# Optimization experiments

Hardware: AMD Instinct MI355X
Metric: run time of the kernel (lower is better)

Reference implementation:

```python
import jax, jax.numpy as jnp
import numpy as np

B, S, D, H, DFF = 4, 1024, 1024, 16, 4096
DK = D // H
EPS = 1e-9


def _layernorm(x, alpha, bias):
    # Faithful to source: torch.std is unbiased (ddof=1), eps added to std.
    mean = jnp.mean(x, axis=-1, keepdims=True)
    xc = x - mean
    std = jnp.sqrt(jnp.sum(xc * xc, axis=-1, keepdims=True) / (x.shape[-1] - 1))
    return alpha * xc / (std + EPS) + bias


def _mha(x, wq_w, wq_b, wo_w, wo_b):
    # Source bug preserved: w_q is used for q, k, AND v projections.
    p = (x @ wq_w + wq_b).reshape(B, S, H, DK).transpose(0, 2, 1, 3)  # [B,H,S,DK]
    scores = jnp.einsum('bhqd,bhkd->bhqk', p, p) / jnp.sqrt(jnp.asarray(DK, x.dtype))
    attn = jax.nn.softmax(scores, axis=-1)
    out = jnp.einsum('bhqk,bhkd->bhqd', attn, p)
    out = out.transpose(0, 2, 1, 3).reshape(B, S, D)
    return out @ wo_w + wo_b


def _ffn(x, w1, b1, w2, b2):
    return jax.nn.relu(x @ w1 + b1) @ w2 + b2


def setup_inputs() -> dict:
    key = jax.random.key(0)
    ks = jax.random.split(key, 8)
    sc = 0.02
    return {
        'x': jax.random.normal(ks[0], (B, S, D), jnp.float32),
        'wq_w': sc * jax.random.normal(ks[1], (D, D), jnp.float32),
        'wq_b': jnp.zeros((D,), jnp.float32),
        'wo_w': sc * jax.random.normal(ks[2], (D, D), jnp.float32),
        'wo_b': jnp.zeros((D,), jnp.float32),
        'ff1_w': sc * jax.random.normal(ks[3], (D, DFF), jnp.float32),
        'ff1_b': jnp.zeros((DFF,), jnp.float32),
        'ff2_w': sc * jax.random.normal(ks[4], (DFF, D), jnp.float32),
        'ff2_b': jnp.zeros((D,), jnp.float32),
        'alpha1': jnp.ones((1,), jnp.float32), 'bias1': jnp.zeros((1,), jnp.float32),
        'alpha2': jnp.ones((1,), jnp.float32), 'bias2': jnp.zeros((1,), jnp.float32),
        'alpha3': jnp.ones((1,), jnp.float32), 'bias3': jnp.zeros((1,), jnp.float32),
    }


def reference(x, wq_w, wq_b, wo_w, wo_b, ff1_w, ff1_b, ff2_w, ff2_b,
              alpha1, bias1, alpha2, bias2, alpha3, bias3):
    h1 = x + _mha(_layernorm(x, alpha1, bias1), wq_w, wq_b, wo_w, wo_b)
    h2 = h1 + _ffn(_layernorm(h1, alpha2, bias2), ff1_w, ff1_b, ff2_w, ff2_b)
    return _layernorm(h2, alpha3, bias3)
```

## Files before the change

kernel.cpp:

```cpp
#include <hip/hip_runtime.h>

typedef short short8 __attribute__((ext_vector_type(8)));
typedef float f32x4 __attribute__((ext_vector_type(4)));
typedef unsigned short u16x4 __attribute__((ext_vector_type(4)));

#define DEV static __device__ __forceinline__

DEV float b2f(unsigned short u) { return __uint_as_float(((unsigned)u) << 16); }
DEV unsigned short f2b(float f) {
    unsigned u = __float_as_uint(f);
    u += 0x7FFFu + ((u >> 16) & 1u);
    return (unsigned short)(u >> 16);
}
DEV unsigned pack2(float a, float b) {
    return (unsigned)f2b(a) | ((unsigned)f2b(b) << 16);
}
DEV float wred_sum(float v) {
#pragma unroll
    for (int o = 32; o; o >>= 1) v += __shfl_xor(v, o);
    return v;
}

DEV void gld_lds16(const unsigned short* g, unsigned short* l) {
    __builtin_amdgcn_global_load_lds((const __attribute__((address_space(1))) void*)g,
                                     (__attribute__((address_space(3))) void*)l, 16, 0, 0);
}

template <bool OUT_BF16>
__global__ __launch_bounds__(256) void ln_kernel(const float* __restrict__ in,
                                                 void* __restrict__ out_v,
                                                 const float* __restrict__ alpha_p,
                                                 const float* __restrict__ bias_p) {
    __shared__ float redA[4], redB[4];
    const int row = blockIdx.x;
    const int t = threadIdx.x;
    const int lane = t & 63, w = t >> 6;

    f32x4 xv = *(const f32x4*)&in[(size_t)row * 1024 + t * 4];

    float s = wred_sum(xv[0] + xv[1] + xv[2] + xv[3]);
    if (lane == 0) redA[w] = s;
    __syncthreads();
    float mean = (redA[0] + redA[1] + redA[2] + redA[3]) * (1.0f / 1024.0f);

    float d0 = xv[0] - mean, d1 = xv[1] - mean, d2 = xv[2] - mean, d3 = xv[3] - mean;
    float ss = wred_sum(d0 * d0 + d1 * d1 + d2 * d2 + d3 * d3);
    if (lane == 0) redB[w] = ss;
    __syncthreads();
    float var = (redB[0] + redB[1] + redB[2] + redB[3]) * (1.0f / 1023.0f);
    float denom = sqrtf(var) + 1e-9f;
    float inv = alpha_p[0] / denom;
    float bias = bias_p[0];

    if (OUT_BF16) {
        u16x4 o;
        o[0] = f2b(d0 * inv + bias);
        o[1] = f2b(d1 * inv + bias);
        o[2] = f2b(d2 * inv + bias);
        o[3] = f2b(d3 * inv + bias);
        *(u16x4*)&((unsigned short*)out_v)[(size_t)row * 1024 + t * 4] = o;
    } else {
        f32x4 o;
        o[0] = d0 * inv + bias;
        o[1] = d1 * inv + bias;
        o[2] = d2 * inv + bias;
        o[3] = d3 * inv + bias;
        *(f32x4*)&((float*)out_v)[(size_t)row * 1024 + t * 4] = o;
    }
}

__global__ __launch_bounds__(256) void transpose_cast_kernel(const float* __restrict__ in,
                                                             unsigned short* __restrict__ out,
                                                             int R, int C) {
    __shared__ unsigned short tile[32][33];
    const int c0 = blockIdx.x * 32, r0 = blockIdx.y * 32;
    const int x = threadIdx.x, y0 = threadIdx.y;
#pragma unroll
    for (int yy = y0; yy < 32; yy += 8) tile[yy][x] = f2b(in[(size_t)(r0 + yy) * C + c0 + x]);
    __syncthreads();
#pragma unroll
    for (int yy = y0; yy < 32; yy += 8) out[(size_t)(c0 + yy) * R + r0 + x] = tile[x][yy];
}

__global__ __launch_bounds__(256) void transpose_bf16_batch(const unsigned short* __restrict__ in,
                                                            unsigned short* __restrict__ out) {
    __shared__ unsigned short tile[32][33];
    const int b = blockIdx.z;
    const int d0 = blockIdx.x * 32, s0 = blockIdx.y * 32;
    const unsigned short* I = in + (size_t)b * 1024 * 1024;
    unsigned short* O = out + (size_t)b * 1024 * 1024;
    const int x = threadIdx.x, y0 = threadIdx.y;
#pragma unroll
    for (int yy = y0; yy < 32; yy += 8) tile[yy][x] = I[(size_t)(s0 + yy) * 1024 + d0 + x];
    __syncthreads();
#pragma unroll
    for (int yy = y0; yy < 32; yy += 8) O[(size_t)(d0 + yy) * 1024 + s0 + x] = tile[x][yy];
}

template <int BM, int BN, bool RELU, bool RES, bool OUT_BF16>
__global__ __launch_bounds__(256) void gemm2(const unsigned short* __restrict__ A,
                                             const unsigned short* __restrict__ Bt,
                                             const float* __restrict__ bias,
                                             const float* __restrict__ res,
                                             void* __restrict__ C_v,
                                             int M, int N, int K) {
    constexpr int WM = BM / 2, WN = BN / 2;
    constexpr int FM = WM / 16, FN = WN / 16;
    __shared__ __align__(16) unsigned short As[BM * 64];
    __shared__ __align__(16) unsigned short Bs[BN * 64];

    const int t = threadIdx.x;
    const int lane = t & 63, w = t >> 6;
    const int wr = w >> 1, wc = w & 1;
    const int lr = lane & 15, g = lane >> 4;

    const int nwg = gridDim.x;
    const int cpx = nwg >> 3;
    const int wg = blockIdx.x;
    const int swz = (wg & 7) * cpx + (wg >> 3);
    const int NB = N / BN;
    const int m0 = (swz / NB) * BM, n0 = (swz % NB) * BN;

    f32x4 acc[FM][FN];
#pragma unroll
    for (int i = 0; i < FM; ++i)
#pragma unroll
        for (int j = 0; j < FN; ++j) acc[i][j] = (f32x4)0.0f;

    for (int k0 = 0; k0 < K; k0 += 64) {
        __syncthreads();
#pragma unroll
        for (int i = 0; i < BM / 32; ++i) {
            int id = i * 256 + t;
            int row = id >> 3, ch = id & 7;
            gld_lds16(&A[(size_t)(m0 + row) * K + k0 + ((ch ^ (row & 7)) * 8)],
                      &As[(size_t)(i * 256 + (t & ~63)) * 8]);
        }
#pragma unroll
        for (int i = 0; i < BN / 32; ++i) {
            int id = i * 256 + t;
            int row = id >> 3, ch = id & 7;
            gld_lds16(&Bt[(size_t)(n0 + row) * K + k0 + ((ch ^ (row & 7)) * 8)],
                      &Bs[(size_t)(i * 256 + (t & ~63)) * 8]);
        }
        __syncthreads();

        short8 af[FM][2], bfr[FN][2];
#pragma unroll
        for (int mi = 0; mi < FM; ++mi) {
            int row = wr * WM + mi * 16 + lr;
#pragma unroll
            for (int ks = 0; ks < 2; ++ks) {
                int ch = (ks * 4 + g) ^ (row & 7);
                af[mi][ks] = *(const short8*)&As[row * 64 + ch * 8];
            }
        }
#pragma unroll
        for (int ni = 0; ni < FN; ++ni) {
            int row = wc * WN + ni * 16 + lr;
#pragma unroll
            for (int ks = 0; ks < 2; ++ks) {
                int ch = (ks * 4 + g) ^ (row & 7);
                bfr[ni][ks] = *(const short8*)&Bs[row * 64 + ch * 8];
            }
        }
#pragma unroll
        for (int ks = 0; ks < 2; ++ks)
#pragma unroll
            for (int mi = 0; mi < FM; ++mi)
#pragma unroll
                for (int ni = 0; ni < FN; ++ni)
                    acc[mi][ni] = __builtin_amdgcn_mfma_f32_16x16x32_bf16(af[mi][ks], bfr[ni][ks], acc[mi][ni], 0, 0, 0);
    }

    const int lg = g;
#pragma unroll
    for (int ni = 0; ni < FN; ++ni) {
        int col = n0 + wc * WN + ni * 16 + lr;
        float bv = bias[col];
#pragma unroll
        for (int mi = 0; mi < FM; ++mi) {
            int row0 = m0 + wr * WM + mi * 16 + lg * 4;
#pragma unroll
            for (int i = 0; i < 4; ++i) {
                int row = row0 + i;
                float x = acc[mi][ni][i] + bv;
                if (RES) x += res[(size_t)row * N + col];
                if (RELU) x = fmaxf(x, 0.0f);
                if (OUT_BF16)
                    ((unsigned short*)C_v)[(size_t)row * N + col] = f2b(x);
                else
                    ((float*)C_v)[(size_t)row * N + col] = x;
            }
        }
    }
}

__global__ __launch_bounds__(256) void attn_mfma_kernel(const unsigned short* __restrict__ p,
                                                        const unsigned short* __restrict__ pT,
                                                        unsigned short* __restrict__ out) {
    __shared__ __align__(16) unsigned short Ks[64 * 64];
    __shared__ __align__(16) unsigned short Vt[64 * 64];
    __shared__ __align__(16) unsigned short Ps[4 * 16 * 64];

    const int t = threadIdx.x;
    const int lane = t & 63, w = t >> 6;
    const int lr = lane & 15, g = lane >> 4;
    const int bh = blockIdx.x;
    const int qblk = blockIdx.y;
    const int b = bh >> 4, h = bh & 15;

    const unsigned short* Pm = p + (size_t)b * (1024 * 1024) + h * 64;
    const unsigned short* PT = pT + (size_t)b * (1024 * 1024) + (size_t)(h * 64) * 1024;

    const int q0 = qblk * 64 + w * 16;
    short8 qa0 = *(const short8*)&Pm[(size_t)(q0 + lr) * 1024 + g * 8];
    short8 qa1 = *(const short8*)&Pm[(size_t)(q0 + lr) * 1024 + 32 + g * 8];

    f32x4 acc[4];
#pragma unroll
    for (int i = 0; i < 4; ++i) acc[i] = (f32x4)0.0f;
    float mrow[4] = {-1e30f, -1e30f, -1e30f, -1e30f};
    float lsum[4] = {0.f, 0.f, 0.f, 0.f};

    unsigned short* Pw = &Ps[w * 16 * 64];

    for (int kt = 0; kt < 16; ++kt) {
        const int key0 = kt * 64;
        __syncthreads();
#pragma unroll
        for (int i = 0; i < 2; ++i) {
            int id = t + i * 256;
            int row = id >> 3, ch = (id & 7) * 8;
            int sw = ch ^ ((row & 7) << 3);
            short8 kv = *(const short8*)&Pm[(size_t)(key0 + row) * 1024 + ch];
            *(short8*)&Ks[row * 64 + sw] = kv;
            short8 vv = *(const short8*)&PT[(size_t)row * 1024 + key0 + ch];
            *(short8*)&Vt[row * 64 + sw] = vv;
        }
        __syncthreads();

        f32x4 s_acc[4];
#pragma unroll
        for (int kg = 0; kg < 4; ++kg) {
            s_acc[kg] = (f32x4)0.0f;
            int krow = kg * 16 + lr;
            int swz = (krow & 7) << 3;
            short8 kb0 = *(const short8*)&Ks[krow * 64 + ((g * 8) ^ swz)];
            short8 kb1 = *(const short8*)&Ks[krow * 64 + ((32 + g * 8) ^ swz)];
            s_acc[kg] = __builtin_amdgcn_mfma_f32_16x16x32_bf16(qa0, kb0, s_acc[kg], 0, 0, 0);
            s_acc[kg] = __builtin_amdgcn_mfma_f32_16x16x32_bf16(qa1, kb1, s_acc[kg], 0, 0, 0);
        }

#pragma unroll
        for (int reg = 0; reg < 4; ++reg) {
            float mx = fmaxf(fmaxf(s_acc[0][reg], s_acc[1][reg]),
                             fmaxf(s_acc[2][reg], s_acc[3][reg])) * 0.125f;
            mx = fmaxf(mx, __shfl_xor(mx, 1));
            mx = fmaxf(mx, __shfl_xor(mx, 2));
            mx = fmaxf(mx, __shfl_xor(mx, 4));
            mx = fmaxf(mx, __shfl_xor(mx, 8));
            float mnew = fmaxf(mrow[reg], mx);
            float scale = __expf(mrow[reg] - mnew);
            mrow[reg] = mnew;
            float psum = 0.f;
#pragma unroll
            for (int kg = 0; kg < 4; ++kg) {
                float pv = __expf(s_acc[kg][reg] * 0.125f - mnew);
                s_acc[kg][reg] = pv;
                psum += pv;
            }
            psum += __shfl_xor(psum, 1);
            psum += __shfl_xor(psum, 2);
            psum += __shfl_xor(psum, 4);
            psum += __shfl_xor(psum, 8);
            lsum[reg] = lsum[reg] * scale + psum;
#pragma unroll
            for (int dg = 0; dg < 4; ++dg) acc[dg][reg] *= scale;
        }

#pragma unroll
        for (int reg = 0; reg < 4; ++reg) {
            int q = g * 4 + reg;
            int swz = (q & 7) << 3;
#pragma unroll
            for (int kg = 0; kg < 4; ++kg) {
                int key = lr + 16 * kg;
                Pw[q * 64 + (key ^ swz)] = f2b(s_acc[kg][reg]);
            }
        }
        int pswz = (lr & 7) << 3;
        short8 pa0 = *(const short8*)&Pw[lr * 64 + ((g * 8) ^ pswz)];
        short8 pa1 = *(const short8*)&Pw[lr * 64 + ((32 + g * 8) ^ pswz)];

#pragma unroll
        for (int dg = 0; dg < 4; ++dg) {
            int drow = dg * 16 + lr;
            int swz = (drow & 7) << 3;
            short8 vb0 = *(const short8*)&Vt[drow * 64 + ((g * 8) ^ swz)];
            short8 vb1 = *(const short8*)&Vt[drow * 64 + ((32 + g * 8) ^ swz)];
            acc[dg] = __builtin_amdgcn_mfma_f32_16x16x32_bf16(pa0, vb0, acc[dg], 0, 0, 0);
            acc[dg] = __builtin_amdgcn_mfma_f32_16x16x32_bf16(pa1, vb1, acc[dg], 0, 0, 0);
        }
    }

    unsigned short* O = out + (size_t)b * (1024 * 1024) + h * 64;
#pragma unroll
    for (int reg = 0; reg < 4; ++reg) {
        float inv = 1.0f / lsum[reg];
        int q = q0 + g * 4 + reg;
#pragma unroll
        for (int dg = 0; dg < 4; ++dg) {
            O[(size_t)q * 1024 + dg * 16 + lr] = f2b(acc[dg][reg] * inv);
        }
    }
}

extern "C" void kernel_launch(void* const* d_in, const int* in_sizes, int n_in,
                              void* d_out, int out_size, void* d_ws, size_t ws_size,
                              hipStream_t stream) {
    const float* x = (const float*)d_in[0];
    const float* wq_w = (const float*)d_in[1];
    const float* wq_b = (const float*)d_in[2];
    const float* wo_w = (const float*)d_in[3];
    const float* wo_b = (const float*)d_in[4];
    const float* ff1_w = (const float*)d_in[5];
    const float* ff1_b = (const float*)d_in[6];
    const float* ff2_w = (const float*)d_in[7];
    const float* ff2_b = (const float*)d_in[8];
    const float* alpha1 = (const float*)d_in[9];
    const float* bias1 = (const float*)d_in[10];
    const float* alpha2 = (const float*)d_in[11];
    const float* bias2 = (const float*)d_in[12];
    const float* alpha3 = (const float*)d_in[13];
    const float* bias3 = (const float*)d_in[14];
    float* out = (float*)d_out;

    const size_t MB = 1u << 20;
    char* ws = (char*)d_ws;
    unsigned short* wq_t = (unsigned short*)(ws + 0 * MB);
    unsigned short* wo_t = (unsigned short*)(ws + 2 * MB);
    unsigned short* ff1_t = (unsigned short*)(ws + 4 * MB);
    unsigned short* ff2_t = (unsigned short*)(ws + 12 * MB);
    unsigned short* lnbuf = (unsigned short*)(ws + 20 * MB);
    unsigned short* pbuf = (unsigned short*)(ws + 28 * MB);
    unsigned short* attn = (unsigned short*)(ws + 36 * MB);
    float* h1 = (float*)(ws + 44 * MB);
    unsigned short* pbT = (unsigned short*)(ws + 60 * MB);
    unsigned short* mid = (unsigned short*)(ws + 60 * MB);
    float* h2 = (float*)(ws + 28 * MB);

    const int M = 4096;

    transpose_cast_kernel<<<dim3(32, 32), dim3(32, 8), 0, stream>>>(wq_w, wq_t, 1024, 1024);
    transpose_cast_kernel<<<dim3(32, 32), dim3(32, 8), 0, stream>>>(wo_w, wo_t, 1024, 1024);
    transpose_cast_kernel<<<dim3(128, 32), dim3(32, 8), 0, stream>>>(ff1_w, ff1_t, 1024, 4096);
    transpose_cast_kernel<<<dim3(32, 128), dim3(32, 8), 0, stream>>>(ff2_w, ff2_t, 4096, 1024);

    ln_kernel<true><<<M, 256, 0, stream>>>(x, lnbuf, alpha1, bias1);
    gemm2<128, 64, false, false, true><<<512, 256, 0, stream>>>(lnbuf, wq_t, wq_b, nullptr, pbuf, M, 1024, 1024);
    transpose_bf16_batch<<<dim3(32, 32, 4), dim3(32, 8), 0, stream>>>(pbuf, pbT);
    attn_mfma_kernel<<<dim3(64, 16), 256, 0, stream>>>(pbuf, pbT, attn);
    gemm2<128, 64, false, true, false><<<512, 256, 0, stream>>>(attn, wo_t, wo_b, x, h1, M, 1024, 1024);
    ln_kernel<true><<<M, 256, 0, stream>>>(h1, lnbuf, alpha2, bias2);
    gemm2<128, 128, true, false, true><<<1024, 256, 0, stream>>>(lnbuf, ff1_t, ff1_b, nullptr, mid, M, 4096, 1024);
    gemm2<128, 64, false, true, false><<<512, 256, 0, stream>>>(mid, ff2_t, ff2_b, h1, h2, M, 1024, 4096);
    ln_kernel<false><<<M, 256, 0, stream>>>(h2, out, alpha3, bias3);
}
```

Before: 258.8 us.

## Add 256x256-tile 512-thread GEMM with 4-buffer LDS pipeline for FF1

Adds a new gemm3 kernel that computes 256x256 output tiles with 8 waves, each holding an 8x4 grid of MFMA accumulators. Operands go straight from global memory into a 4-slot LDS ring with XOR-swizzled chunks, two stages of prefetch, and waits on a partial vmcnt. It also swizzles the workgroup order and raises wave priority around the MFMA block. The FF1 projection (4096x4096x1024, bias+ReLU, bf16 out) now uses it instead of gemm2 with 128x128 tiles, for more data reuse per load and better overlap of loads with compute. The cost is high register pressure, 128KB of LDS per block, and only 256 workgroups.

```diff
diff --git a/kernel.cpp b/kernel.cpp
--- a/kernel.cpp
+++ b/kernel.cpp
@@ -11,9 +11,6 @@
     unsigned u = __float_as_uint(f);
     u += 0x7FFFu + ((u >> 16) & 1u);
     return (unsigned short)(u >> 16);
-}
-DEV unsigned pack2(float a, float b) {
-    return (unsigned)f2b(a) | ((unsigned)f2b(b) << 16);
 }
 DEV float wred_sum(float v) {
 #pragma unroll
@@ -186,6 +183,114 @@
                 int row = row0 + i;
                 float x = acc[mi][ni][i] + bv;
                 if (RES) x += res[(size_t)row * N + col];
+                if (RELU) x = fmaxf(x, 0.0f);
+                if (OUT_BF16)
+                    ((unsigned short*)C_v)[(size_t)row * N + col] = f2b(x);
+                else
+                    ((float*)C_v)[(size_t)row * N + col] = x;
+            }
+        }
+    }
+}
+
+template <bool RELU, bool OUT_BF16>
+__global__ __launch_bounds__(512, 2) void gemm3(const unsigned short* __restrict__ A,
+                                                const unsigned short* __restrict__ Bt,
+                                                const float* __restrict__ bias,
+                                                void* __restrict__ C_v,
+                                                int M, int N, int K) {
+    __shared__ __align__(16) unsigned short As[4][256 * 32];
+    __shared__ __align__(16) unsigned short Bs[4][256 * 32];
+
+    const int t = threadIdx.x;
+    const int lane = t & 63;
+    const int wid = t >> 6;
+    const int wr = wid >> 2, wc = wid & 3;
+    const int lr = lane & 15, g = lane >> 4;
+
+    const int nwg = gridDim.x;
+    const int cpx = nwg >> 3;
+    const int wg = blockIdx.x;
+    const int swz = (wg & 7) * cpx + (wg >> 3);
+    const int NB = N / 256;
+    const int m0 = (swz / NB) * 256, n0 = (swz % NB) * 256;
+
+    f32x4 acc[8][4];
+#pragma unroll
+    for (int i = 0; i < 8; ++i)
+#pragma unroll
+        for (int j = 0; j < 4; ++j) acc[i][j] = (f32x4)0.0f;
+
+    const int NT = K / 32;
+
+#define STAGE3(kt)                                                                          \
+    {                                                                                       \
+        const int buf_ = (kt) & 3;                                                          \
+        const int k0_ = (kt) * 32;                                                          \
+        _Pragma("unroll") for (int s = 0; s < 2; ++s) {                                     \
+            int id = s * 512 + t;                                                           \
+            int row = id >> 2;                                                              \
+            int ch = (id & 3) ^ ((row >> 1) & 3);                                           \
+            gld_lds16(&A[(size_t)(m0 + row) * K + k0_ + ch * 8],                            \
+                      &As[buf_][(size_t)(s * 512 + (t & ~63)) * 8]);                        \
+            gld_lds16(&Bt[(size_t)(n0 + row) * K + k0_ + ch * 8],                           \
+                      &Bs[buf_][(size_t)(s * 512 + (t & ~63)) * 8]);                        \
+        }                                                                                   \
+    }
+
+    STAGE3(0);
+    STAGE3(1);
+    asm volatile("s_waitcnt vmcnt(4)" ::: "memory");
+    __builtin_amdgcn_sched_barrier(0);
+    __builtin_amdgcn_s_barrier();
+
+    for (int kt = 0; kt < NT; ++kt) {
+        const int buf = kt & 3;
+        if (kt + 2 < NT) STAGE3(kt + 2);
+
+        short8 af[8], bf[4];
+#pragma unroll
+        for (int mi = 0; mi < 8; ++mi) {
+            int row = wr * 128 + mi * 16 + lr;
+            int ch = g ^ ((row >> 1) & 3);
+            af[mi] = *(const short8*)&As[buf][row * 32 + ch * 8];
+        }
+#pragma unroll
+        for (int nj = 0; nj < 4; ++nj) {
+            int row = wc * 64 + nj * 16 + lr;
+            int ch = g ^ ((row >> 1) & 3);
+            bf[nj] = *(const short8*)&Bs[buf][row * 32 + ch * 8];
+        }
+
+        __builtin_amdgcn_s_setprio(1);
+#pragma unroll
+        for (int mi = 0; mi < 8; ++mi)
+#pragma unroll
+            for (int nj = 0; nj < 4; ++nj)
+                acc[mi][nj] = __builtin_amdgcn_mfma_f32_16x16x32_bf16(af[mi], bf[nj], acc[mi][nj], 0, 0, 0);
+        __builtin_amdgcn_s_setprio(0);
+
+        if (kt + 2 < NT) {
+            asm volatile("s_waitcnt vmcnt(4)" ::: "memory");
+        } else if (kt + 1 < NT) {
+            asm volatile("s_waitcnt vmcnt(0)" ::: "memory");
+        }
+        __builtin_amdgcn_sched_barrier(0);
+        __builtin_amdgcn_s_barrier();
+    }
+#undef STAGE3
+
+#pragma unroll
+    for (int nj = 0; nj < 4; ++nj) {
+        int col = n0 + wc * 64 + nj * 16 + lr;
+        float bv = bias[col];
+#pragma unroll
+        for (int mi = 0; mi < 8; ++mi) {
+            int row0 = m0 + wr * 128 + mi * 16 + g * 4;
+#pragma unroll
+            for (int i = 0; i < 4; ++i) {
+                int row = row0 + i;
+                float x = acc[mi][nj][i] + bv;
                 if (RELU) x = fmaxf(x, 0.0f);
                 if (OUT_BF16)
                     ((unsigned short*)C_v)[(size_t)row * N + col] = f2b(x);
@@ -363,7 +468,7 @@
     attn_mfma_kernel<<<dim3(64, 16), 256, 0, stream>>>(pbuf, pbT, attn);
     gemm2<128, 64, false, true, false><<<512, 256, 0, stream>>>(attn, wo_t, wo_b, x, h1, M, 1024, 1024);
     ln_kernel<true><<<M, 256, 0, stream>>>(h1, lnbuf, alpha2, bias2);
-    gemm2<128, 128, true, false, true><<<1024, 256, 0, stream>>>(lnbuf, ff1_t, ff1_b, nullptr, mid, M, 4096, 1024);
+    gemm3<true, true><<<256, 512, 0, stream>>>(lnbuf, ff1_t, ff1_b, mid, M, 4096, 1024);
     gemm2<128, 64, false, true, false><<<512, 256, 0, stream>>>(mid, ff2_t, ff2_b, h1, h2, M, 1024, 4096);
     ln_kernel<false><<<M, 256, 0, stream>>>(h2, out, alpha3, bias3);
 }
```

Result: no change. 254.5 us (-1.7%).
